# Performance work log

Measured on AMD Instinct MI355X. Metric: run time of the kernel, lower is better.

## Reference

```python
import jax, jax.numpy as jnp
import numpy as np

B, T, C, H = 16, 512, 256, 8
HS_T = C // H   # temporal head size = 32
HS_S = T // H   # spatial head size = 64
EPS = 1e-6


def _ln(x, w, b):
    m = x.mean(-1, keepdims=True)
    v = ((x - m) ** 2).mean(-1, keepdims=True)
    return (x - m) / jnp.sqrt(v + EPS) * w + b


def setup_inputs() -> dict:
    key = jax.random.key(0)
    ks = jax.random.split(key, 16)
    rn = lambda k, s, scale: jax.random.normal(k, s, dtype=jnp.float32) * scale
    inp = {
        "x_T": rn(ks[0], (B, T, C), 1.0),
        "x_S": rn(ks[1], (B, C, T), 1.0),
        # temporal attention: per-head q/k/v projections, stacked [H, hs, C]
        "Wq_t": rn(ks[2], (H, HS_T, C), C ** -0.5),
        "Wk_t": rn(ks[3], (H, HS_T, C), C ** -0.5),
        "Wv_t": rn(ks[4], (H, HS_T, C), C ** -0.5),
        "Wo": rn(ks[5], (C, C), C ** -0.5),
        # spatial attention: per-head q/k over the time axis, stacked [H, hs_s, T]
        "Wq_s": rn(ks[6], (H, HS_S, T), T ** -0.5),
        "Wk_s": rn(ks[7], (H, HS_S, T), T ** -0.5),
        # feed-forward blocks (expansion_factor=4)
        "ff1_w1": rn(ks[8], (4 * C, C), C ** -0.5),
        "ff1_b1": jnp.zeros((4 * C,), jnp.float32),
        "ff1_w2": rn(ks[9], (C, 4 * C), (4 * C) ** -0.5),
        "ff1_b2": jnp.zeros((C,), jnp.float32),
        "ff2_w1": rn(ks[10], (4 * C, C), C ** -0.5),
        "ff2_b1": jnp.zeros((4 * C,), jnp.float32),
        "ff2_w2": rn(ks[11], (C, 4 * C), (4 * C) ** -0.5),
        "ff2_b2": jnp.zeros((C,), jnp.float32),
        # layernorm affine params
        "t_ln1_w": jnp.ones((C,), jnp.float32), "t_ln1_b": jnp.zeros((C,), jnp.float32),
        "t_ln2_w": jnp.ones((C,), jnp.float32), "t_ln2_b": jnp.zeros((C,), jnp.float32),
        "s_ln1_w": jnp.ones((T,), jnp.float32), "s_ln1_b": jnp.zeros((T,), jnp.float32),
        "fus_ln_w": jnp.ones((C,), jnp.float32), "fus_ln_b": jnp.zeros((C,), jnp.float32),
    }
    return inp


def reference(x_T, x_S, Wq_t, Wk_t, Wv_t, Wo, Wq_s, Wk_s,
              ff1_w1, ff1_b1, ff1_w2, ff1_b2, ff2_w1, ff2_b1, ff2_w2, ff2_b2,
              t_ln1_w, t_ln1_b, t_ln2_w, t_ln2_b, s_ln1_w, s_ln1_b,
              fus_ln_w, fus_ln_b):
    # ---- temporal (causal) multi-head attention ----
    h = _ln(x_T, t_ln1_w, t_ln1_b)                         # [B,T,C]
    q = jnp.einsum('btc,hdc->bhtd', h, Wq_t)
    k = jnp.einsum('btc,hdc->bhtd', h, Wk_t)
    v = jnp.einsum('btc,hdc->bhtd', h, Wv_t)
    scores = jnp.einsum('bhtd,bhsd->bhts', q, k) / jnp.sqrt(jnp.float32(HS_T))
    causal = jnp.tril(jnp.ones((T, T), dtype=bool))
    scores = jnp.where(causal, scores, -jnp.inf)
    att = jax.nn.softmax(scores, axis=-1)
    o = jnp.einsum('bhts,bhsd->bhtd', att, v)              # [B,H,T,hs]
    o = o.transpose(0, 2, 1, 3).reshape(B, T, C)           # concat heads
    attn_out = o @ Wo.T
    x = x_T + attn_out
    # FFN 1
    h2 = _ln(x, t_ln2_w, t_ln2_b)
    f = jax.nn.relu(h2 @ ff1_w1.T + ff1_b1) @ ff1_w2.T + ff1_b2
    temporal_out = x + f                                   # [B,T,C]
    # ---- spatial (non-causal) attention over neurons ----
    hs = _ln(x_S, s_ln1_w, s_ln1_b)                        # [B,C,T]
    qs = jnp.einsum('bct,hdt->bhcd', hs, Wq_s)
    ks = jnp.einsum('bct,hdt->bhcd', hs, Wk_s)
    sc = jnp.einsum('bhcd,bhed->bhce', qs, ks) / jnp.sqrt(jnp.float32(HS_S))
    spatial_weights = jax.nn.softmax(sc, axis=-1).mean(axis=1)   # [B,C,C], mean over heads
    # ---- fusion ----
    fused = jnp.einsum('bce,bte->btc', spatial_weights, temporal_out)
    x2 = temporal_out + fused
    h3 = _ln(x2, fus_ln_w, fus_ln_b)
    f2 = jax.nn.relu(h3 @ ff2_w1.T + ff2_b1) @ ff2_w2.T + ff2_b2
    out = x2 + f2
    return out, spatial_weights
```

## Files before the change

kernel.cpp:

```cpp
#include <hip/hip_runtime.h>
#include <hip/hip_bf16.h>

typedef __hip_bfloat16 bf16;
typedef __attribute__((ext_vector_type(8))) short short8;
typedef __attribute__((ext_vector_type(4))) float f32x4;

#define F_BIAS 1
#define F_RELU 2
#define F_RES  4

__device__ __forceinline__ void st_out(float* p, float v){ *p = v; }
__device__ __forceinline__ void st_out(bf16* p, float v){ *p = __float2bfloat16(v); }
__device__ __forceinline__ short f2bs(float f){
  bf16 h = __float2bfloat16(f);
  return *reinterpret_cast<short*>(&h);
}

__device__ __forceinline__ void gl_lds16(const void* g, void* l){
  __builtin_amdgcn_global_load_lds(
      (const __attribute__((address_space(1))) void*)g,
      (__attribute__((address_space(3))) void*)l, 16, 0, 0);
}

__device__ __forceinline__ void lgkm_barrier(){
  asm volatile("s_waitcnt lgkmcnt(0)" ::: "memory");
  __builtin_amdgcn_s_barrier();
}


struct ProArgs {
  const float* wsrc[10];
  bf16* wdst[10];
  const float *xT, *xS, *tl1w, *tl1b, *sl1w, *sl1b;
  bf16 *hT, *hS;
};

template<int RL>
__device__ __forceinline__ void wave_ln(bf16* __restrict__ dst,
    const float* __restrict__ src, const float* __restrict__ w,
    const float* __restrict__ bvec, int row){
  int lane = threadIdx.x & 63;
  const float* s = src + (size_t)row*RL;
  float4 v0 = *(const float4*)(s + lane*4);
  float4 v1 = {0.f,0.f,0.f,0.f};
  float sum = v0.x+v0.y+v0.z+v0.w;
  float sq  = v0.x*v0.x+v0.y*v0.y+v0.z*v0.z+v0.w*v0.w;
  if (RL == 512){
    v1 = *(const float4*)(s + 256 + lane*4);
    sum += v1.x+v1.y+v1.z+v1.w;
    sq  += v1.x*v1.x+v1.y*v1.y+v1.z*v1.z+v1.w*v1.w;
  }
  #pragma unroll
  for (int off=32; off; off>>=1){
    sum += __shfl_xor(sum, off, 64);
    sq  += __shfl_xor(sq , off, 64);
  }
  const float inv = 1.0f/(float)RL;
  float mean = sum*inv;
  float rstd = rsqrtf(sq*inv - mean*mean + 1e-6f);
  float4 w0 = *(const float4*)(w + lane*4);
  float4 b0 = *(const float4*)(bvec + lane*4);
  bf16* d = dst + (size_t)row*RL;
  short4 o;
  o.x = f2bs((v0.x-mean)*rstd*w0.x + b0.x);
  o.y = f2bs((v0.y-mean)*rstd*w0.y + b0.y);
  o.z = f2bs((v0.z-mean)*rstd*w0.z + b0.z);
  o.w = f2bs((v0.w-mean)*rstd*w0.w + b0.w);
  *(short4*)((short*)d + lane*4) = o;
  if (RL == 512){
    float4 w1 = *(const float4*)(w + 256 + lane*4);
    float4 b1 = *(const float4*)(bvec + 256 + lane*4);
    short4 o1;
    o1.x = f2bs((v1.x-mean)*rstd*w1.x + b1.x);
    o1.y = f2bs((v1.y-mean)*rstd*w1.y + b1.y);
    o1.z = f2bs((v1.z-mean)*rstd*w1.z + b1.z);
    o1.w = f2bs((v1.w-mean)*rstd*w1.w + b1.w);
    *(short4*)((short*)d + 256 + lane*4) = o1;
  }
}

__global__ __launch_bounds__(256) void prologue(ProArgs a){
  int blk = blockIdx.x;
  int wid = threadIdx.x >> 6;
  if (blk < 1792){
    int v = blk*256 + threadIdx.x;
    int e = v*4;
    int seg = (e>=65536)+(e>=131072)+(e>=196608)+(e>=262144)+(e>=524288)
            + (e>=786432)+(e>=1048576)+(e>=1310720)+(e>=1572864);
    const int starts[10] = {0,65536,131072,196608,262144,524288,786432,
                            1048576,1310720,1572864};
    int off = e - starts[seg];
    float4 f = *(const float4*)(a.wsrc[seg] + off);
    short4 o;
    o.x = f2bs(f.x); o.y = f2bs(f.y); o.z = f2bs(f.z); o.w = f2bs(f.w);
    if (seg >= 3 && seg <= 7){
      int ldlog = (seg==5 || seg==7) ? 10 : 8;
      int r  = off >> ldlog;
      int c  = off & ((1<<ldlog)-1);
      int tn = r >> 4, lr = r & 15;
      int tk = c >> 5, qd = (c>>3)&3, b = c&7;
      int nkt = 1 << (ldlog-5);
      int dst = (((tn*nkt + tk)*64) + qd*16 + lr)*8 + b;
      *(short4*)((short*)a.wdst[seg] + dst) = o;
    } else {
      *(short4*)((short*)a.wdst[seg] + off) = o;
    }
  } else if (blk < 1792 + 2048){
    wave_ln<256>(a.hT, a.xT, a.tl1w, a.tl1b, (blk-1792)*4 + wid);
  } else {
    wave_ln<512>(a.hS, a.xS, a.sl1w, a.sl1b, (blk-3840)*4 + wid);
  }
}

template<int BM, int BN, int BK>
__device__ __forceinline__ void gemm_body(
    short* __restrict__ AsB, short* __restrict__ BsB,
    const bf16* __restrict__ A, const bf16* __restrict__ B,
    float* __restrict__ outF, bf16* __restrict__ outB,
    const float* __restrict__ bias, const float* __restrict__ resid,
    int K, int lda, int ldb, int ldc, int flags, int m0, int n0){
  int tid = threadIdx.x;
  int w = tid>>6, lane = tid&63, quad = lane>>4, l16 = lane&15;
  constexpr int MF  = BM/32;
  constexpr int NF  = BN/32;
  constexpr int CPR = BK/8;
  constexpr int CA  = BM*CPR/256;
  constexpr int CB  = BN*CPR/256;
  int wm = (w>>1)*(BM/2), wn = (w&1)*(BN/2);
  f32x4 acc[MF][NF];
  #pragma unroll
  for (int r=0;r<MF;r++)
    #pragma unroll
    for (int j=0;j<NF;j++)
      acc[r][j] = (f32x4){0.f,0.f,0.f,0.f};

  auto stage = [&](int k0, int half){
    short* as = AsB + half*(BM*BK);
    short* bs = BsB + half*(BN*BK);
    #pragma unroll
    for (int c=0;c<CA;c++){
      int ch = tid + c*256;
      int row = ch / CPR, p = ch % CPR;
      gl_lds16(A + (size_t)(m0+row)*lda + k0 + ((p ^ (row&(CPR-1)))*8),
               &as[row*BK + p*8]);
    }
    #pragma unroll
    for (int c=0;c<CB;c++){
      int ch = tid + c*256;
      int row = ch / CPR, p = ch % CPR;
      gl_lds16(B + (size_t)(n0+row)*ldb + k0 + ((p ^ (row&(CPR-1)))*8),
               &bs[row*BK + p*8]);
    }
  };

  stage(0, 0);
  int nk = K / BK;
  for (int t = 0; t < nk; ++t){
    __syncthreads();
    if (t+1 < nk) stage((t+1)*BK, (t+1)&1);
    const short* as = AsB + (t&1)*(BM*BK);
    const short* bs = BsB + (t&1)*(BN*BK);
    #pragma unroll
    for (int ks=0; ks<BK/32; ++ks){
      short8 af[MF], bfr[NF];
      #pragma unroll
      for (int r=0;r<MF;r++){
        int rr = wm + r*16 + l16;
        af[r] = *(short8*)&as[rr*BK + (((ks*4+quad) ^ (rr&(CPR-1)))*8)];
      }
      #pragma unroll
      for (int j=0;j<NF;j++){
        int rr = wn + j*16 + l16;
        bfr[j] = *(short8*)&bs[rr*BK + (((ks*4+quad) ^ (rr&(CPR-1)))*8)];
      }
      #pragma unroll
      for (int r=0;r<MF;r++)
        #pragma unroll
        for (int j=0;j<NF;j++)
          acc[r][j] = __builtin_amdgcn_mfma_f32_16x16x32_bf16(af[r], bfr[j], acc[r][j], 0,0,0);
    }
  }
  #pragma unroll
  for (int r=0;r<MF;r++){
    int mb = m0 + wm + r*16 + quad*4;
    #pragma unroll
    for (int j=0;j<NF;j++){
      int n = n0 + wn + j*16 + l16;
      float bv = (flags & F_BIAS) ? bias[n] : 0.0f;
      #pragma unroll
      for (int e=0;e<4;e++){
        float v = acc[r][j][e] + bv;
        if (flags & F_RELU) v = fmaxf(v, 0.0f);
        long long idx = (long long)(mb+e)*ldc + n;
        if (flags & F_RES) v += resid[idx];
        if (outF) outF[idx] = v;
        if (outB) st_out(outB + idx, v);
      }
    }
  }
}

struct GArgs {
  const bf16 *A, *B;
  float* outF; bf16* outB;
  const float *bias, *resid;
  int K, lda, ldb, ldc, flags, ty;
};
__global__ __launch_bounds__(256) void gemm_dual(GArgs g0, GArgs g1, int n0){
  __shared__ __align__(16) short As[2*128*64];
  __shared__ __align__(16) short Bs[2*128*64];
  int id = blockIdx.x;
  bool first = id < n0;
  const GArgs& g = first ? g0 : g1;
  int t = first ? id : id - n0;
  int bx = t / g.ty, by = t - bx*g.ty;
  gemm_body<128,128,64>(As, Bs, g.A, g.B, g.outF, g.outB, g.bias, g.resid,
                        g.K, g.lda, g.ldb, g.ldc, g.flags, bx*128, by*128);
}

struct LnFfnArgs {
  const bf16 *A;
  const bf16 *Bm;
  const float *resid0;
  const float *lnw, *lnb;
  const bf16 *W1; const float *B1;
  const bf16 *W2; const float *B2;
  float *outF; bf16 *outB;
  long long sA, sB, sR, sO;
};

__global__ __launch_bounds__(512) void lnffn(LnFfnArgs a){
  __shared__ __align__(16) short Hin[32*256];
  __shared__ __align__(16) short Hs[32*1024];
  float (*redS)[32] = (float(*)[32])Hs;
  float (*redQ)[32] = (float(*)[32])(Hs + 512);
  int bz = blockIdx.z;
  const bf16* A  = a.A  + (size_t)bz*a.sA;
  const bf16* Bm = a.Bm + (size_t)bz*a.sB;
  long long rbase = (long long)bz*a.sR;
  long long obase = (long long)bz*a.sO;
  int tid = threadIdx.x;
  int w = tid>>6, lane = tid&63, quad = lane>>4, l16 = lane&15;
  int m0 = blockIdx.x*32;
  int mt0 = m0 >> 4;

  f32x4 acc0[2][2];
  #pragma unroll
  for (int r=0;r<2;r++)
    #pragma unroll
    for (int j=0;j<2;j++) acc0[r][j] = (f32x4){0.f,0.f,0.f,0.f};
  #pragma unroll
  for (int ks=0; ks<8; ++ks){
    short8 af[2], bk[2];
    #pragma unroll
    for (int r=0;r<2;r++)
      af[r] = *(const short8*)(A + (((size_t)(mt0+r)*8 + ks)*64 + lane)*8);
    #pragma unroll
    for (int j=0;j<2;j++){
      int tile = w*2 + j;
      bk[j] = *(const short8*)(Bm + ((size_t)(tile*8 + ks)*64 + lane)*8);
    }
    #pragma unroll
    for (int r=0;r<2;r++)
      #pragma unroll
      for (int j=0;j<2;j++)
        acc0[r][j] = __builtin_amdgcn_mfma_f32_16x16x32_bf16(af[r], bk[j], acc0[r][j], 0,0,0);
  }
  #pragma unroll
  for (int r=0;r<2;r++)
    #pragma unroll
    for (int e=0;e<4;e++){
      int row = r*16 + quad*4 + e;
      float s = 0.f, q2 = 0.f;
      #pragma unroll
      for (int j=0;j<2;j++){
        float v = acc0[r][j][e] +
                  a.resid0[rbase + (long long)(m0+row)*256 + w*32 + j*16 + l16];
        acc0[r][j][e] = v;
        s += v; q2 += v*v;
      }
      #pragma unroll
      for (int off=1; off<16; off<<=1){
        s  += __shfl_xor(s , off, 16);
        q2 += __shfl_xor(q2, off, 16);
      }
      if (l16==0){ redS[w][row] = s; redQ[w][row] = q2; }
    }
  __syncthreads();
  #pragma unroll
  for (int r=0;r<2;r++)
    #pragma unroll
    for (int e=0;e<4;e++){
      int row = r*16 + quad*4 + e;
      float tot = 0.f, tq = 0.f;
      #pragma unroll
      for (int ww=0; ww<8; ww++){ tot += redS[ww][row]; tq += redQ[ww][row]; }
      float mean = tot * (1.0f/256.0f);
      float var  = tq * (1.0f/256.0f) - mean*mean;
      float rstd = rsqrtf(var + 1e-6f);
      #pragma unroll
      for (int j=0;j<2;j++){
        int col = w*32 + j*16 + l16;
        float h = (acc0[r][j][e]-mean)*rstd*a.lnw[col] + a.lnb[col];
        int g = col >> 3;
        Hin[row*256 + ((g ^ row)*8) + (col&7)] = f2bs(h);
      }
    }
  __syncthreads();

  for (int hc=0; hc<2; ++hc){
    f32x4 acc1[2][4];
    #pragma unroll
    for (int r=0;r<2;r++)
      #pragma unroll
      for (int j=0;j<4;j++) acc1[r][j] = (f32x4){0.f,0.f,0.f,0.f};
    #pragma unroll
    for (int ks=0; ks<8; ++ks){
      short8 af[2], bk[4];
      #pragma unroll
      for (int r=0;r<2;r++){
        int rr = r*16 + l16;
        int kk = ks*4 + quad;
        af[r] = *(short8*)&Hin[rr*256 + ((kk ^ rr)*8)];
      }
      #pragma unroll
      for (int j=0;j<4;j++){
        int ht = w*8 + hc*4 + j;
        bk[j] = *(const short8*)(a.W1 + ((size_t)(ht*8 + ks)*64 + lane)*8);
      }
      #pragma unroll
      for (int r=0;r<2;r++)
        #pragma unroll
        for (int j=0;j<4;j++)
          acc1[r][j] = __builtin_amdgcn_mfma_f32_16x16x32_bf16(af[r], bk[j], acc1[r][j], 0,0,0);
    }
    #pragma unroll
    for (int r=0;r<2;r++)
      #pragma unroll
      for (int j=0;j<4;j++)
        #pragma unroll
        for (int e=0;e<4;e++){
          int row = r*16 + quad*4 + e;
          int col = w*128 + hc*64 + j*16 + l16;
          float v = fmaxf(acc1[r][j][e] + a.B1[col], 0.0f);
          int g = col>>3;
          Hs[row*1024 + ((g ^ (row&7))*8) + (col&7)] = f2bs(v);
        }
  }
  __syncthreads();

  f32x4 accB[2][2];
  #pragma unroll
  for (int r=0;r<2;r++)
    #pragma unroll
    for (int j=0;j<2;j++) accB[r][j] = (f32x4){0.f,0.f,0.f,0.f};
  #pragma unroll 8
  for (int ks=0; ks<32; ++ks){
    short8 af[2], bk[2];
    #pragma unroll
    for (int r=0;r<2;r++){
      int rr = r*16 + l16;
      int kk = ks*4 + quad;
      af[r] = *(short8*)&Hs[rr*1024 + ((kk ^ (rr&7))*8)];
    }
    #pragma unroll
    for (int j=0;j<2;j++){
      int nt = w*2 + j;
      bk[j] = *(const short8*)(a.W2 + ((size_t)(nt*32 + ks)*64 + lane)*8);
    }
    #pragma unroll
    for (int r=0;r<2;r++)
      #pragma unroll
      for (int j=0;j<2;j++)
        accB[r][j] = __builtin_amdgcn_mfma_f32_16x16x32_bf16(af[r], bk[j], accB[r][j], 0,0,0);
  }
  #pragma unroll
  for (int r=0;r<2;r++)
    #pragma unroll
    for (int j=0;j<2;j++){
      int n = w*32 + j*16 + l16;
      float bv = a.B2[n];
      #pragma unroll
      for (int e=0;e<4;e++){
        int row = r*16 + quad*4 + e;
        long long idx = obase + (long long)(m0+row)*256 + n;
        float v = accB[r][j][e] + bv + acc0[r][j][e];
        a.outF[idx] = v;
        if (a.outB){
          long long grow = (long long)(m0+row);
          long long pdst = (grow>>9)*131072
                         + (((grow&511)>>4)*8 + (n>>5))*512
                         + ((n>>3)&3)*128 + (grow&15)*8 + (n&7);
          st_out(a.outB + pdst, v);
        }
      }
    }
}

__device__ __forceinline__ int fsw(int row){ return (row>>1)&3; }
__global__ __launch_bounds__(256) void flash_mfma(
    const bf16* __restrict__ qkv, bf16* __restrict__ o){
  int qt = (int)gridDim.x - 1 - (int)blockIdx.x;
  int h = blockIdx.y, b = blockIdx.z;
  int tid = threadIdx.x;
  int w = tid>>6, lane = tid&63, quad = lane>>4, l16 = lane&15;
  __shared__ __align__(16) bf16 Qs[64*32];
  __shared__ __align__(16) bf16 Ks[2][64*32];
  __shared__ __align__(16) bf16 Vt[2][32*72];
  __shared__ __align__(16) bf16 Ps[64*72];
  const bf16* base = qkv + (size_t)b*512*768;
  int t0 = qt*64;
  int srow = tid>>2, spos = tid&3;
  gl_lds16(base + (size_t)(t0+srow)*768 + h*32 + ((spos ^ fsw(srow))*8),
           &Qs[srow*32 + spos*8]);
  {
    const bf16* rp = base + (size_t)srow*768 + h*32;
    gl_lds16(rp + 256 + ((spos ^ fsw(srow))*8), &Ks[0][srow*32 + spos*8]);
    short8 v = *(const short8*)(rp + 512 + spos*8);
    #pragma unroll
    for (int q=0;q<8;q++){
      short tmp = v[q];
      Vt[0][(spos*8+q)*72 + srow] = *(bf16*)&tmp;
    }
  }
  f32x4 accO[2];
  accO[0] = (f32x4){0.f,0.f,0.f,0.f};
  accO[1] = (f32x4){0.f,0.f,0.f,0.f};
  float m_i[4], l_i[4];
  #pragma unroll
  for (int e=0;e<4;e++){ m_i[e] = -3.0e38f; l_i[e] = 0.0f; }
  const float scale = 0.17677669529663687f;
  __syncthreads();
  int rq = w*16 + l16;
  short8 aq = *(short8*)&Qs[rq*32 + ((quad ^ fsw(rq))*8)];

  for (int kt = 0; kt <= qt; ++kt){
    if (kt) __syncthreads();
    int cur = kt&1, nxt = cur^1;
    bool pre = (kt < qt);
    short8 vpre;
    if (pre){
      const bf16* rp = base + (size_t)((kt+1)*64 + srow)*768 + h*32;
      gl_lds16(rp + 256 + ((spos ^ fsw(srow))*8), &Ks[nxt][srow*32 + spos*8]);
      vpre = *(const short8*)(rp + 512 + spos*8);
    }
    f32x4 S[4];
    #pragma unroll
    for (int j2=0;j2<4;j2++){
      int rk = j2*16 + l16;
      short8 bk = *(short8*)&Ks[cur][rk*32 + ((quad ^ fsw(rk))*8)];
      S[j2] = __builtin_amdgcn_mfma_f32_16x16x32_bf16(aq, bk,
                (f32x4){0.f,0.f,0.f,0.f}, 0,0,0);
    }
    bool diag = (kt == qt);
    int s0 = kt*64;
    int qrow_base = t0 + w*16 + quad*4;
    #pragma unroll
    for (int e=0;e<4;e++){
      float sv[4];
      #pragma unroll
      for (int j2=0;j2<4;j2++){
        float x = S[j2][e]*scale;
        if (diag && (s0 + j2*16 + l16 > qrow_base + e)) x = -3.0e38f;
        sv[j2] = x;
      }
      float mx = fmaxf(fmaxf(sv[0],sv[1]), fmaxf(sv[2],sv[3]));
      #pragma unroll
      for (int off=1; off<16; off<<=1) mx = fmaxf(mx, __shfl_xor(mx, off, 64));
      float m_new = fmaxf(m_i[e], mx);
      float alpha = __expf(m_i[e]-m_new);
      float rs = 0.0f;
      #pragma unroll
      for (int j2=0;j2<4;j2++){
        float p = __expf(sv[j2]-m_new);
        rs += p;
        Ps[(w*16+quad*4+e)*72 + j2*16 + l16] = __float2bfloat16(p);
      }
      #pragma unroll
      for (int off=1; off<16; off<<=1) rs += __shfl_xor(rs, off, 64);
      l_i[e] = l_i[e]*alpha + rs;
      m_i[e] = m_new;
      accO[0][e] *= alpha;
      accO[1][e] *= alpha;
    }
    asm volatile("s_waitcnt lgkmcnt(0)" ::: "memory");
    __builtin_amdgcn_sched_barrier(0);
    #pragma unroll
    for (int sh=0; sh<2; ++sh){
      short8 ap = *(short8*)&Ps[(w*16+l16)*72 + sh*32 + quad*8];
      #pragma unroll
      for (int dh=0; dh<2; ++dh){
        short8 bv = *(short8*)&Vt[cur][(dh*16+l16)*72 + sh*32 + quad*8];
        accO[dh] = __builtin_amdgcn_mfma_f32_16x16x32_bf16(ap, bv, accO[dh], 0,0,0);
      }
    }
    if (pre){
      #pragma unroll
      for (int q=0;q<8;q++){
        short tmp = vpre[q];
        Vt[nxt][(spos*8+q)*72 + srow] = *(bf16*)&tmp;
      }
    }
  }
  {
    long long fr = ((long long)b*32 + qt*4 + w)*8 + h;
    #pragma unroll
    for (int e=0;e<4;e++){
      float inv = 1.0f/l_i[e];
      long long rb8 = fr*512 + (quad*4+e)*8 + (l16&7);
      o[rb8 + (l16>>3)*128]       = __float2bfloat16(accO[0][e]*inv);
      o[rb8 + (2+(l16>>3))*128]   = __float2bfloat16(accO[1][e]*inv);
    }
  }
}

__global__ __launch_bounds__(256) void spatial_fused(
    const bf16* __restrict__ qk, float* __restrict__ out1,
    bf16* __restrict__ swB){
  int ct = blockIdx.x & 15, b = blockIdx.x >> 4;
  int tid = threadIdx.x;
  int w = tid>>6, lane = tid&63, quad = lane>>4, l16 = lane&15;
  __shared__ __align__(16) bf16 Qall[16*512];
  __shared__ __align__(16) bf16 Ks[2][256*64];
  __shared__ float redM[4][16], redS2[4][16];
  const bf16* qbase = qk + ((size_t)(b*256 + ct*16))*1024;
  #pragma unroll
  for (int c=0;c<4;c++){
    int ch = tid + c*256;
    int row = ch>>6, p = ch&63;
    gl_lds16(qbase + (size_t)row*1024 + ((p ^ (row&7))*8), &Qall[row*512 + p*8]);
  }
  auto stageK = [&](int h, int half){
    bf16* ks = Ks[half];
    #pragma unroll
    for (int c=0;c<8;c++){
      int ch = tid + c*256;
      int e = ch>>3, p = ch&7;
      gl_lds16(qk + ((size_t)(b*256 + e))*1024 + 512 + h*64 + ((p ^ (e&7))*8),
               &ks[e*64 + p*8]);
    }
  };
  stageK(0, 0);
  float fRes[4][4];
  #pragma unroll
  for (int j=0;j<4;j++)
    #pragma unroll
    for (int e=0;e<4;e++) fRes[j][e] = 0.0f;

  for (int h=0; h<8; ++h){
    __syncthreads();
    if (h+1 < 8) stageK(h+1, (h+1)&1);
    const bf16* kcur = Ks[h&1];
    f32x4 acc[4];
    #pragma unroll
    for (int j=0;j<4;j++) acc[j] = (f32x4){0.f,0.f,0.f,0.f};
    #pragma unroll
    for (int ki=0; ki<2; ++ki){
      int g = h*8 + ki*4 + quad;
      short8 aq = *(short8*)&Qall[l16*512 + ((g ^ (l16&7))*8)];
      #pragma unroll
      for (int j=0;j<4;j++){
        int e = w*64 + j*16 + l16;
        short8 bk = *(short8*)&kcur[e*64 + (((ki*4+quad) ^ (e&7))*8)];
        acc[j] = __builtin_amdgcn_mfma_f32_16x16x32_bf16(aq, bk, acc[j], 0,0,0);
      }
    }
    #pragma unroll
    for (int e=0;e<4;e++){
      float m = -3.0e38f;
      #pragma unroll
      for (int j=0;j<4;j++){
        float s = acc[j][e]*0.125f;
        acc[j][e] = s;
        m = fmaxf(m, s);
      }
      #pragma unroll
      for (int off=1; off<16; off<<=1) m = fmaxf(m, __shfl_xor(m, off, 16));
      if (l16==0) redM[w][quad*4+e] = m;
    }
    lgkm_barrier();
    #pragma unroll
    for (int e=0;e<4;e++){
      int r = quad*4+e;
      float m = fmaxf(fmaxf(redM[0][r],redM[1][r]), fmaxf(redM[2][r],redM[3][r]));
      float s = 0.0f;
      #pragma unroll
      for (int j=0;j<4;j++){
        float p = __expf(acc[j][e]-m);
        acc[j][e] = p; s += p;
      }
      #pragma unroll
      for (int off=1; off<16; off<<=1) s += __shfl_xor(s, off, 16);
      if (l16==0) redS2[w][r] = s;
    }
    lgkm_barrier();
    #pragma unroll
    for (int e=0;e<4;e++){
      int r = quad*4+e;
      float tot = redS2[0][r]+redS2[1][r]+redS2[2][r]+redS2[3][r];
      float inv = 0.125f/tot;
      #pragma unroll
      for (int j=0;j<4;j++) fRes[j][e] += acc[j][e]*inv;
    }
  }
  #pragma unroll
  for (int e=0;e<4;e++){
    int c = ct*16 + quad*4 + e;
    size_t rb = ((size_t)b*256 + c)*256;
    #pragma unroll
    for (int j=0;j<4;j++){
      int col = w*64 + j*16 + l16;
      out1[rb+col] = fRes[j][e];
      size_t pdst = (size_t)b*65536
                  + ((size_t)(ct*8 + (col>>5)))*512
                  + ((col>>3)&3)*128 + (c&15)*8 + (col&7);
      swB[pdst] = __float2bfloat16(fRes[j][e]);
    }
  }
}

extern "C" void kernel_launch(void* const* d_in, const int* in_sizes, int n_in,
                              void* d_out, int out_size, void* d_ws, size_t ws_size,
                              hipStream_t stream){
  (void)in_sizes; (void)n_in; (void)out_size; (void)ws_size;
  const float* x_T  = (const float*)d_in[0];
  const float* x_S  = (const float*)d_in[1];
  const float* Wq_t = (const float*)d_in[2];
  const float* Wk_t = (const float*)d_in[3];
  const float* Wv_t = (const float*)d_in[4];
  const float* Wo   = (const float*)d_in[5];
  const float* Wq_s = (const float*)d_in[6];
  const float* Wk_s = (const float*)d_in[7];
  const float* f1w1 = (const float*)d_in[8];
  const float* f1b1 = (const float*)d_in[9];
  const float* f1w2 = (const float*)d_in[10];
  const float* f1b2 = (const float*)d_in[11];
  const float* f2w1 = (const float*)d_in[12];
  const float* f2b1 = (const float*)d_in[13];
  const float* f2w2 = (const float*)d_in[14];
  const float* f2b2 = (const float*)d_in[15];
  const float* tl1w = (const float*)d_in[16];
  const float* tl1b = (const float*)d_in[17];
  const float* tl2w = (const float*)d_in[18];
  const float* tl2b = (const float*)d_in[19];
  const float* sl1w = (const float*)d_in[20];
  const float* sl1b = (const float*)d_in[21];
  const float* flw  = (const float*)d_in[22];
  const float* flb  = (const float*)d_in[23];

  float* ws = (float*)d_ws;
  size_t off = 0;
  bf16*  Wqkvb  = (bf16*)(ws + off); off += 768*256/2;
  bf16*  Wob    = (bf16*)(ws + off); off += 256*256/2;
  bf16*  f1w1b  = (bf16*)(ws + off); off += 1024*256/2;
  bf16*  f1w2b  = (bf16*)(ws + off); off += 256*1024/2;
  bf16*  f2w1b  = (bf16*)(ws + off); off += 1024*256/2;
  bf16*  f2w2b  = (bf16*)(ws + off); off += 256*1024/2;
  bf16*  WSb    = (bf16*)(ws + off); off += 1024*512/2;
  bf16*  bufHb  = (bf16*)(ws + off); off += (size_t)8192*256/2;
  bf16*  bufHSb = (bf16*)(ws + off); off += (size_t)4096*512/2;
  bf16*  bufQKVb= (bf16*)(ws + off); off += (size_t)8192*768/2;
  bf16*  bufOb  = (bf16*)(ws + off); off += (size_t)8192*256/2;
  bf16*  bufTOb = (bf16*)(ws + off); off += (size_t)8192*256/2;
  bf16*  swB    = (bf16*)(ws + off); off += (size_t)16*256*256/2;
  bf16*  qkB    = (bf16*)(ws + off); off += (size_t)4096*1024/2;
  float* bufTO  = ws + off; off += (size_t)8192*256;

  float* out0 = (float*)d_out;
  float* out1 = out0 + (size_t)16*512*256;

  ProArgs pa;
  pa.wsrc[0]=Wq_t;  pa.wdst[0]=Wqkvb;
  pa.wsrc[1]=Wk_t;  pa.wdst[1]=Wqkvb+65536;
  pa.wsrc[2]=Wv_t;  pa.wdst[2]=Wqkvb+131072;
  pa.wsrc[3]=Wo;    pa.wdst[3]=Wob;
  pa.wsrc[4]=f1w1;  pa.wdst[4]=f1w1b;
  pa.wsrc[5]=f1w2;  pa.wdst[5]=f1w2b;
  pa.wsrc[6]=f2w1;  pa.wdst[6]=f2w1b;
  pa.wsrc[7]=f2w2;  pa.wdst[7]=f2w2b;
  pa.wsrc[8]=Wq_s;  pa.wdst[8]=WSb;
  pa.wsrc[9]=Wk_s;  pa.wdst[9]=WSb+262144;
  pa.xT=x_T; pa.xS=x_S; pa.tl1w=tl1w; pa.tl1b=tl1b;
  pa.sl1w=sl1w; pa.sl1b=sl1b; pa.hT=bufHb; pa.hS=bufHSb;
  prologue<<<4864,256,0,stream>>>(pa);

  GArgs gq, gs;
  gq.A=bufHb;  gq.B=Wqkvb; gq.outF=nullptr; gq.outB=bufQKVb;
  gq.bias=nullptr; gq.resid=nullptr;
  gq.K=256; gq.lda=256; gq.ldb=256; gq.ldc=768; gq.flags=0; gq.ty=6;
  gs.A=bufHSb; gs.B=WSb;   gs.outF=nullptr; gs.outB=qkB;
  gs.bias=nullptr; gs.resid=nullptr;
  gs.K=512; gs.lda=512; gs.ldb=512; gs.ldc=1024; gs.flags=0; gs.ty=8;
  gemm_dual<<<640,256,0,stream>>>(gq, gs, 384);

  spatial_fused<<<256,256,0,stream>>>(qkB, out1, swB);

  flash_mfma<<<dim3(8,8,16),256,0,stream>>>(bufQKVb, bufOb);

  LnFfnArgs la1;
  la1.A=bufOb; la1.Bm=Wob;
  la1.resid0=x_T; la1.lnw=tl2w; la1.lnb=tl2b;
  la1.W1=f1w1b; la1.B1=f1b1; la1.W2=f1w2b; la1.B2=f1b2;
  la1.outF=bufTO; la1.outB=bufTOb;
  la1.sA=0; la1.sB=0; la1.sR=0; la1.sO=0;
  lnffn<<<dim3(256,1,1),512,0,stream>>>(la1);

  LnFfnArgs la2;
  la2.A=bufTOb; la2.Bm=swB;
  la2.resid0=bufTO; la2.lnw=flw; la2.lnb=flb;
  la2.W1=f2w1b; la2.B1=f2b1; la2.W2=f2w2b; la2.B2=f2b2;
  la2.outF=out0; la2.outB=nullptr;
  la2.sA=131072; la2.sB=65536; la2.sR=131072; la2.sO=131072;
  lnffn<<<dim3(16,1,16),512,0,stream>>>(la2);
}
```

Before: 254.7 us.

## Fuse temporal FFN and fusion FFN into one kernel keeping activations on-chip

Merges the two lnffn launches into a single kernel. Each 32-row block computes the Wo projection with LN and FFN1, writes temporal_out to LDS as bf16, then multiplies by the spatial weights, applies LN and FFN2 without leaving the block. This removes the global round trip of temporal_out (fp32 and packed bf16 buffers) and one kernel launch. The cost is a longer kernel with more serialized phases and barriers per block, and the spatial GEMM now reads its A operand from LDS.

New measurement: 248.0 us. 2.6% less time.

```diff
diff --git a/kernel.cpp b/kernel.cpp
--- a/kernel.cpp
+++ b/kernel.cpp
@@ -218,96 +218,25 @@
                         g.K, g.lda, g.ldb, g.ldc, g.flags, bx*128, by*128);
 }
 
-struct LnFfnArgs {
+struct L2XArgs {
   const bf16 *A;
-  const bf16 *Bm;
-  const float *resid0;
-  const float *lnw, *lnb;
-  const bf16 *W1; const float *B1;
-  const bf16 *W2; const float *B2;
-  float *outF; bf16 *outB;
-  long long sA, sB, sR, sO;
+  const bf16 *Wo;
+  const float *xT;
+  const float *ln1w, *ln1b;
+  const bf16 *W1a; const float *B1a;
+  const bf16 *W2a; const float *B2a;
+  const bf16 *sw;
+  const float *ln2w, *ln2b;
+  const bf16 *W1b; const float *B1b;
+  const bf16 *W2b; const float *B2b;
+  float *out0;
 };
 
-__global__ __launch_bounds__(512) void lnffn(LnFfnArgs a){
-  __shared__ __align__(16) short Hin[32*256];
-  __shared__ __align__(16) short Hs[32*1024];
-  float (*redS)[32] = (float(*)[32])Hs;
-  float (*redQ)[32] = (float(*)[32])(Hs + 512);
-  int bz = blockIdx.z;
-  const bf16* A  = a.A  + (size_t)bz*a.sA;
-  const bf16* Bm = a.Bm + (size_t)bz*a.sB;
-  long long rbase = (long long)bz*a.sR;
-  long long obase = (long long)bz*a.sO;
-  int tid = threadIdx.x;
-  int w = tid>>6, lane = tid&63, quad = lane>>4, l16 = lane&15;
-  int m0 = blockIdx.x*32;
-  int mt0 = m0 >> 4;
-
-  f32x4 acc0[2][2];
-  #pragma unroll
-  for (int r=0;r<2;r++)
-    #pragma unroll
-    for (int j=0;j<2;j++) acc0[r][j] = (f32x4){0.f,0.f,0.f,0.f};
-  #pragma unroll
-  for (int ks=0; ks<8; ++ks){
-    short8 af[2], bk[2];
-    #pragma unroll
-    for (int r=0;r<2;r++)
-      af[r] = *(const short8*)(A + (((size_t)(mt0+r)*8 + ks)*64 + lane)*8);
-    #pragma unroll
-    for (int j=0;j<2;j++){
-      int tile = w*2 + j;
-      bk[j] = *(const short8*)(Bm + ((size_t)(tile*8 + ks)*64 + lane)*8);
-    }
-    #pragma unroll
-    for (int r=0;r<2;r++)
-      #pragma unroll
-      for (int j=0;j<2;j++)
-        acc0[r][j] = __builtin_amdgcn_mfma_f32_16x16x32_bf16(af[r], bk[j], acc0[r][j], 0,0,0);
-  }
-  #pragma unroll
-  for (int r=0;r<2;r++)
-    #pragma unroll
-    for (int e=0;e<4;e++){
-      int row = r*16 + quad*4 + e;
-      float s = 0.f, q2 = 0.f;
-      #pragma unroll
-      for (int j=0;j<2;j++){
-        float v = acc0[r][j][e] +
-                  a.resid0[rbase + (long long)(m0+row)*256 + w*32 + j*16 + l16];
-        acc0[r][j][e] = v;
-        s += v; q2 += v*v;
-      }
-      #pragma unroll
-      for (int off=1; off<16; off<<=1){
-        s  += __shfl_xor(s , off, 16);
-        q2 += __shfl_xor(q2, off, 16);
-      }
-      if (l16==0){ redS[w][row] = s; redQ[w][row] = q2; }
-    }
-  __syncthreads();
-  #pragma unroll
-  for (int r=0;r<2;r++)
-    #pragma unroll
-    for (int e=0;e<4;e++){
-      int row = r*16 + quad*4 + e;
-      float tot = 0.f, tq = 0.f;
-      #pragma unroll
-      for (int ww=0; ww<8; ww++){ tot += redS[ww][row]; tq += redQ[ww][row]; }
-      float mean = tot * (1.0f/256.0f);
-      float var  = tq * (1.0f/256.0f) - mean*mean;
-      float rstd = rsqrtf(var + 1e-6f);
-      #pragma unroll
-      for (int j=0;j<2;j++){
-        int col = w*32 + j*16 + l16;
-        float h = (acc0[r][j][e]-mean)*rstd*a.lnw[col] + a.lnb[col];
-        int g = col >> 3;
-        Hin[row*256 + ((g ^ row)*8) + (col&7)] = f2bs(h);
-      }
-    }
-  __syncthreads();
-
+__device__ __forceinline__ void ffn_block(
+    short* Hin, short* Hs,
+    const bf16* W1, const float* B1, const bf16* W2, const float* B2,
+    int w, int quad, int l16, int lane,
+    f32x4 resid[2][2], f32x4 outv[2][2]){
   for (int hc=0; hc<2; ++hc){
     f32x4 acc1[2][4];
     #pragma unroll
@@ -326,7 +255,7 @@
       #pragma unroll
       for (int j=0;j<4;j++){
         int ht = w*8 + hc*4 + j;
-        bk[j] = *(const short8*)(a.W1 + ((size_t)(ht*8 + ks)*64 + lane)*8);
+        bk[j] = *(const short8*)(W1 + ((size_t)(ht*8 + ks)*64 + lane)*8);
       }
       #pragma unroll
       for (int r=0;r<2;r++)
@@ -342,13 +271,12 @@
         for (int e=0;e<4;e++){
           int row = r*16 + quad*4 + e;
           int col = w*128 + hc*64 + j*16 + l16;
-          float v = fmaxf(acc1[r][j][e] + a.B1[col], 0.0f);
+          float v = fmaxf(acc1[r][j][e] + B1[col], 0.0f);
           int g = col>>3;
           Hs[row*1024 + ((g ^ (row&7))*8) + (col&7)] = f2bs(v);
         }
   }
   __syncthreads();
-
   f32x4 accB[2][2];
   #pragma unroll
   for (int r=0;r<2;r++)
@@ -366,7 +294,7 @@
     #pragma unroll
     for (int j=0;j<2;j++){
       int nt = w*2 + j;
-      bk[j] = *(const short8*)(a.W2 + ((size_t)(nt*32 + ks)*64 + lane)*8);
+      bk[j] = *(const short8*)(W2 + ((size_t)(nt*32 + ks)*64 + lane)*8);
     }
     #pragma unroll
     for (int r=0;r<2;r++)
@@ -379,20 +307,159 @@
     #pragma unroll
     for (int j=0;j<2;j++){
       int n = w*32 + j*16 + l16;
-      float bv = a.B2[n];
+      float bv = B2[n];
+      #pragma unroll
+      for (int e=0;e<4;e++)
+        outv[r][j][e] = accB[r][j][e] + bv + resid[r][j][e];
+    }
+}
+
+__global__ __launch_bounds__(512) void lnffn2x(L2XArgs a){
+  __shared__ __align__(16) short Hin[32*256];
+  __shared__ __align__(16) short Hs[32*1024];
+  float (*redS)[32] = (float(*)[32])Hs;
+  float (*redQ)[32] = (float(*)[32])(Hs + 512);
+  int tid = threadIdx.x;
+  int w = tid>>6, lane = tid&63, quad = lane>>4, l16 = lane&15;
+  int m0 = blockIdx.x*32;
+  int mt0 = m0 >> 4;
+  int bz = blockIdx.x >> 4;
+  const bf16* swb = a.sw + (size_t)bz*65536;
+
+  auto ln_to_hin = [&](f32x4 x[2][2], const float* lw, const float* lb){
+    #pragma unroll
+    for (int r=0;r<2;r++)
       #pragma unroll
       for (int e=0;e<4;e++){
         int row = r*16 + quad*4 + e;
-        long long idx = obase + (long long)(m0+row)*256 + n;
-        float v = accB[r][j][e] + bv + acc0[r][j][e];
-        a.outF[idx] = v;
-        if (a.outB){
-          long long grow = (long long)(m0+row);
-          long long pdst = (grow>>9)*131072
-                         + (((grow&511)>>4)*8 + (n>>5))*512
-                         + ((n>>3)&3)*128 + (grow&15)*8 + (n&7);
-          st_out(a.outB + pdst, v);
+        float s = 0.f, q2 = 0.f;
+        #pragma unroll
+        for (int j=0;j<2;j++){ s += x[r][j][e]; q2 += x[r][j][e]*x[r][j][e]; }
+        #pragma unroll
+        for (int off=1; off<16; off<<=1){
+          s  += __shfl_xor(s , off, 16);
+          q2 += __shfl_xor(q2, off, 16);
         }
+        if (l16==0){ redS[w][row] = s; redQ[w][row] = q2; }
+      }
+    __syncthreads();
+    #pragma unroll
+    for (int r=0;r<2;r++)
+      #pragma unroll
+      for (int e=0;e<4;e++){
+        int row = r*16 + quad*4 + e;
+        float tot = 0.f, tq = 0.f;
+        #pragma unroll
+        for (int ww=0; ww<8; ww++){ tot += redS[ww][row]; tq += redQ[ww][row]; }
+        float mean = tot * (1.0f/256.0f);
+        float var  = tq * (1.0f/256.0f) - mean*mean;
+        float rstd = rsqrtf(var + 1e-6f);
+        #pragma unroll
+        for (int j=0;j<2;j++){
+          int col = w*32 + j*16 + l16;
+          float h = (x[r][j][e]-mean)*rstd*lw[col] + lb[col];
+          int g = col >> 3;
+          Hin[row*256 + ((g ^ row)*8) + (col&7)] = f2bs(h);
+        }
+      }
+    __syncthreads();
+  };
+
+  f32x4 accX[2][2];
+  #pragma unroll
+  for (int r=0;r<2;r++)
+    #pragma unroll
+    for (int j=0;j<2;j++) accX[r][j] = (f32x4){0.f,0.f,0.f,0.f};
+  #pragma unroll
+  for (int ks=0; ks<8; ++ks){
+    short8 af[2], bk[2];
+    #pragma unroll
+    for (int r=0;r<2;r++)
+      af[r] = *(const short8*)(a.A + (((size_t)(mt0+r)*8 + ks)*64 + lane)*8);
+    #pragma unroll
+    for (int j=0;j<2;j++){
+      int tile = w*2 + j;
+      bk[j] = *(const short8*)(a.Wo + ((size_t)(tile*8 + ks)*64 + lane)*8);
+    }
+    #pragma unroll
+    for (int r=0;r<2;r++)
+      #pragma unroll
+      for (int j=0;j<2;j++)
+        accX[r][j] = __builtin_amdgcn_mfma_f32_16x16x32_bf16(af[r], bk[j], accX[r][j], 0,0,0);
+  }
+  #pragma unroll
+  for (int r=0;r<2;r++)
+    #pragma unroll
+    for (int e=0;e<4;e++){
+      int row = r*16 + quad*4 + e;
+      #pragma unroll
+      for (int j=0;j<2;j++)
+        accX[r][j][e] += a.xT[(long long)(m0+row)*256 + w*32 + j*16 + l16];
+    }
+  ln_to_hin(accX, a.ln1w, a.ln1b);
+
+  f32x4 accT[2][2];
+  ffn_block(Hin, Hs, a.W1a, a.B1a, a.W2a, a.B2a, w, quad, l16, lane, accX, accT);
+
+  #pragma unroll
+  for (int r=0;r<2;r++)
+    #pragma unroll
+    for (int j=0;j<2;j++)
+      #pragma unroll
+      for (int e=0;e<4;e++){
+        int row = r*16 + quad*4 + e;
+        int col = w*32 + j*16 + l16;
+        int g = col >> 3;
+        Hin[row*256 + ((g ^ row)*8) + (col&7)] = f2bs(accT[r][j][e]);
+      }
+  __syncthreads();
+
+  f32x4 accX2[2][2];
+  #pragma unroll
+  for (int r=0;r<2;r++)
+    #pragma unroll
+    for (int j=0;j<2;j++) accX2[r][j] = (f32x4){0.f,0.f,0.f,0.f};
+  #pragma unroll
+  for (int ks=0; ks<8; ++ks){
+    short8 af[2], bk[2];
+    #pragma unroll
+    for (int r=0;r<2;r++){
+      int rr = r*16 + l16;
+      int kk = ks*4 + quad;
+      af[r] = *(short8*)&Hin[rr*256 + ((kk ^ rr)*8)];
+    }
+    #pragma unroll
+    for (int j=0;j<2;j++){
+      int tile = w*2 + j;
+      bk[j] = *(const short8*)(swb + ((size_t)(tile*8 + ks)*64 + lane)*8);
+    }
+    #pragma unroll
+    for (int r=0;r<2;r++)
+      #pragma unroll
+      for (int j=0;j<2;j++)
+        accX2[r][j] = __builtin_amdgcn_mfma_f32_16x16x32_bf16(af[r], bk[j], accX2[r][j], 0,0,0);
+  }
+  #pragma unroll
+  for (int r=0;r<2;r++)
+    #pragma unroll
+    for (int j=0;j<2;j++)
+      #pragma unroll
+      for (int e=0;e<4;e++)
+        accX2[r][j][e] += accT[r][j][e];
+  ln_to_hin(accX2, a.ln2w, a.ln2b);
+
+  f32x4 accO[2][2];
+  ffn_block(Hin, Hs, a.W1b, a.B1b, a.W2b, a.B2b, w, quad, l16, lane, accX2, accO);
+
+  #pragma unroll
+  for (int r=0;r<2;r++)
+    #pragma unroll
+    for (int j=0;j<2;j++){
+      int n = w*32 + j*16 + l16;
+      #pragma unroll
+      for (int e=0;e<4;e++){
+        int row = r*16 + quad*4 + e;
+        a.out0[(long long)(m0+row)*256 + n] = accO[r][j][e];
       }
     }
 }
@@ -661,10 +728,8 @@
   bf16*  bufHSb = (bf16*)(ws + off); off += (size_t)4096*512/2;
   bf16*  bufQKVb= (bf16*)(ws + off); off += (size_t)8192*768/2;
   bf16*  bufOb  = (bf16*)(ws + off); off += (size_t)8192*256/2;
-  bf16*  bufTOb = (bf16*)(ws + off); off += (size_t)8192*256/2;
   bf16*  swB    = (bf16*)(ws + off); off += (size_t)16*256*256/2;
   bf16*  qkB    = (bf16*)(ws + off); off += (size_t)4096*1024/2;
-  float* bufTO  = ws + off; off += (size_t)8192*256;
 
   float* out0 = (float*)d_out;
   float* out1 = out0 + (size_t)16*512*256;
@@ -697,19 +762,11 @@
 
   flash_mfma<<<dim3(8,8,16),256,0,stream>>>(bufQKVb, bufOb);
 
-  LnFfnArgs la1;
-  la1.A=bufOb; la1.Bm=Wob;
-  la1.resid0=x_T; la1.lnw=tl2w; la1.lnb=tl2b;
-  la1.W1=f1w1b; la1.B1=f1b1; la1.W2=f1w2b; la1.B2=f1b2;
-  la1.outF=bufTO; la1.outB=bufTOb;
-  la1.sA=0; la1.sB=0; la1.sR=0; la1.sO=0;
-  lnffn<<<dim3(256,1,1),512,0,stream>>>(la1);
-
-  LnFfnArgs la2;
-  la2.A=bufTOb; la2.Bm=swB;
-  la2.resid0=bufTO; la2.lnw=flw; la2.lnb=flb;
-  la2.W1=f2w1b; la2.B1=f2b1; la2.W2=f2w2b; la2.B2=f2b2;
-  la2.outF=out0; la2.outB=nullptr;
-  la2.sA=131072; la2.sB=65536; la2.sR=131072; la2.sO=131072;
-  lnffn<<<dim3(16,1,16),512,0,stream>>>(la2);
-}
+  L2XArgs la;
+  la.A=bufOb; la.Wo=Wob; la.xT=x_T; la.ln1w=tl2w; la.ln1b=tl2b;
+  la.W1a=f1w1b; la.B1a=f1b1; la.W2a=f1w2b; la.B2a=f1b2;
+  la.sw=swB; la.ln2w=flw; la.ln2b=flb;
+  la.W1b=f2w1b; la.B1b=f2b1; la.W2b=f2w2b; la.B2b=f2b2;
+  la.out0=out0;
+  lnffn2x<<<256,512,0,stream>>>(la);
+}
```
